# Performance work log

Measured on AMD Instinct MI355X. Metric: run time of the kernel, lower is better.

Reference implementation:

```python
import jax, jax.numpy as jnp
import numpy as np

N_USERS = 100000
M_ITEMS = 200000
K_DIM = 128
N_BASKET = 50
GAMMA = (1.0, 1.0, 1.0, 1.0)


def setup_inputs() -> dict:
    key = jax.random.key(0)
    k1, k2, k3, k4, k5 = jax.random.split(key, 5)
    n, m, k = N_USERS, M_ITEMS, K_DIM
    p = n + 2 * m
    # Build one transaction x of length 2*p: [target transaction t | t^m transaction]
    rng = np.random.default_rng(0)
    x = np.zeros(2 * p, dtype=np.float32)
    # target transaction t
    x[rng.integers(n)] = 1.0                      # user one-hot
    x[n + rng.integers(m)] = 1.0                  # target item one-hot
    basket = rng.choice(m, size=N_BASKET, replace=False)
    x[n + m + basket] = 1.0                       # basket multi-hot
    # t^m transaction (unused by forward math, present for faithfulness)
    x[p + rng.integers(n)] = 1.0
    x[p + n + rng.integers(m)] = 1.0
    basket2 = rng.choice(m, size=N_BASKET, replace=False)
    x[p + n + m + basket2] = 1.0
    return {
        "x": jnp.asarray(x),
        "delta": jnp.ones((1,), dtype=jnp.float32),
        "pmi": jnp.zeros((1,), dtype=jnp.float32),
        "w_0": jax.random.normal(k1, (1,), dtype=jnp.float32),
        "w_bias": jax.random.normal(k2, (p, 1), dtype=jnp.float32),
        "u_V": jax.random.normal(k3, (n, k), dtype=jnp.float32),
        "t_V": jax.random.normal(k4, (m, k), dtype=jnp.float32),
        "b_V": jax.random.normal(k5, (m, k), dtype=jnp.float32),
    }


def _fm(t, w_0, w_bias, u_V, t_V, b_V):
    n, m = u_V.shape[0], t_V.shape[0]
    xr = t[None, :]                                  # (1, n+2m)
    bias = xr @ w_bias                               # (1, 1)
    u_vec = xr[:, :n] @ u_V                          # (1, k) user latent
    t_vec = xr[:, n:n + m] @ t_V                     # (1, k) target-item latent
    xb = t[n + m:]                                   # (m,) basket multi-hot mask
    s = xb @ b_V                                     # (k,)  sum of selected basket vecs
    sq_sum = jnp.sum(xb @ (b_V * b_V))               # scalar sum_i ||b_i||^2
    u_t = jnp.sum(u_vec * t_vec, axis=-1, keepdims=True)   # (1,1)
    t_b = jnp.sum(t_vec * s, axis=-1, keepdims=True)        # (1,1) sum_i t.b_i
    # closed-form FM pairwise trick: sum_{i<j} b_i.b_j = 0.5*(||sum||^2 - sum ||.||^2)
    bs = 0.5 * (jnp.sum(s * s) - sq_sum)                    # scalar
    u_b = jnp.sum(u_vec * s, axis=-1, keepdims=True)        # (1,1)
    g0, g1, g2, g3 = GAMMA
    return w_0 + bias + g0 * u_t + g1 * t_b + g2 * bs + g3 * u_b


def reference(x, delta, pmi, w_0, w_bias, u_V, t_V, b_V):
    n, m = u_V.shape[0], t_V.shape[0]
    p = n + 2 * m
    t = x[:p]
    y = _fm(t, w_0, w_bias, u_V, t_V, b_V)           # (1,1)
    y = -jax.nn.log_sigmoid(y * delta)
    return y
```

## Files before the change

### kernel.cpp

```cpp
#include <hip/hip_runtime.h>
#include <math.h>

#define N_USERS 100000
#define M_ITEMS 200000
#define K_DIM   128
#define P_DIM   (N_USERS + 2 * M_ITEMS)
#define CAP     1024


__global__ void scan_kernel(const float* __restrict__ x,
                            int* __restrict__ count,
                            int* __restrict__ eidx,
                            float* __restrict__ eval) {
    const int n4 = P_DIM / 4;
    int i4 = blockIdx.x * blockDim.x + threadIdx.x;
    if (i4 >= n4) return;
    float4 v = reinterpret_cast<const float4*>(x)[i4];
    float a0 = v.x, a1 = v.y, a2 = v.z, a3 = v.w;
    if (a0 != 0.0f) { int p = atomicAdd(count, 1); if (p < CAP) { eidx[p] = 4*i4 + 0; eval[p] = a0; } }
    if (a1 != 0.0f) { int p = atomicAdd(count, 1); if (p < CAP) { eidx[p] = 4*i4 + 1; eval[p] = a1; } }
    if (a2 != 0.0f) { int p = atomicAdd(count, 1); if (p < CAP) { eidx[p] = 4*i4 + 2; eval[p] = a2; } }
    if (a3 != 0.0f) { int p = atomicAdd(count, 1); if (p < CAP) { eidx[p] = 4*i4 + 3; eval[p] = a3; } }
}

__global__ void finish_kernel(const int* __restrict__ count,
                              const int* __restrict__ eidx,
                              const float* __restrict__ eval,
                              const float* __restrict__ w0,
                              const float* __restrict__ delta,
                              const float* __restrict__ w_bias,
                              const float* __restrict__ uV,
                              const float* __restrict__ tV,
                              const float* __restrict__ bV,
                              float* __restrict__ out) {
    const int tid = threadIdx.x;
    int cnt = *count;
    if (cnt > CAP) cnt = CAP;

    float u = 0.0f, t = 0.0f, s = 0.0f, sq = 0.0f, bias = 0.0f;
    for (int e = 0; e < cnt; ++e) {
        const int   idx = eidx[e];
        const float val = eval[e];
        if (tid == 0) bias += val * w_bias[idx];
        if (idx < N_USERS) {
            u += val * uV[(size_t)idx * K_DIM + tid];
        } else if (idx < N_USERS + M_ITEMS) {
            t += val * tV[(size_t)(idx - N_USERS) * K_DIM + tid];
        } else {
            float b = bV[(size_t)(idx - N_USERS - M_ITEMS) * K_DIM + tid];
            s  += val * b;
            sq += val * b * b;
        }
    }

    __shared__ float sh[5][K_DIM];
    sh[0][tid] = u * t;
    sh[1][tid] = t * s;
    sh[2][tid] = s * s;
    sh[3][tid] = u * s;
    sh[4][tid] = sq;
    __syncthreads();
    for (int off = K_DIM / 2; off > 0; off >>= 1) {
        if (tid < off) {
            #pragma unroll
            for (int j = 0; j < 5; ++j) sh[j][tid] += sh[j][tid + off];
        }
        __syncthreads();
    }

    if (tid == 0) {
        const float ut = sh[0][0], tb = sh[1][0], ss = sh[2][0],
                    ub = sh[3][0], sqs = sh[4][0];
        const float bs = 0.5f * (ss - sqs);
        float y = w0[0] + bias + ut + tb + bs + ub;
        float z = y * delta[0];
        float a = -z;
        out[0] = fmaxf(a, 0.0f) + log1pf(expf(-fabsf(a)));
    }
}

extern "C" void kernel_launch(void* const* d_in, const int* in_sizes, int n_in,
                              void* d_out, int out_size, void* d_ws, size_t ws_size,
                              hipStream_t stream) {
    const float* x      = (const float*)d_in[0];
    const float* delta  = (const float*)d_in[1];
    const float* w0     = (const float*)d_in[3];
    const float* w_bias = (const float*)d_in[4];
    const float* uV     = (const float*)d_in[5];
    const float* tV     = (const float*)d_in[6];
    const float* bV     = (const float*)d_in[7];
    float* out = (float*)d_out;

    int*   count = (int*)d_ws;
    int*   eidx  = (int*)((char*)d_ws + 16);
    float* eval  = (float*)((char*)d_ws + 16 + CAP * sizeof(int));

    hipMemsetAsync(d_ws, 0, 16, stream);

    const int n4 = P_DIM / 4;
    const int blocks = (n4 + 255) / 256;
    scan_kernel<<<blocks, 256, 0, stream>>>(x, count, eidx, eval);
    finish_kernel<<<1, K_DIM, 0, stream>>>(count, eidx, eval, w0, delta,
                                           w_bias, uV, tV, bV, out);
}
```

Baseline: 250.0 us.

## Compact nonzeros per block in LDS and parallelize gather across 1024 threads

The scan kernel now collects nonzeros into a per-block shared-memory list and writes per-block counts, so the global atomic counter and the memset launch are no longer needed. The finish kernel gathers these per-block lists into shared memory, then splits the embedding-row gathers across 8 slices of 128 threads and computes the bias terms in parallel with a tree reduction. This targets the serial latency chain of the single 128-thread finish loop and removes global atomics. In exchange, the finish kernel must read all per-block counts, and nonzeros beyond the fixed per-block and total caps are dropped.

```diff
diff --git a/kernel.cpp b/kernel.cpp
--- a/kernel.cpp
+++ b/kernel.cpp
@@ -5,74 +5,134 @@
 #define M_ITEMS 200000
 #define K_DIM   128
 #define P_DIM   (N_USERS + 2 * M_ITEMS)
-#define CAP     1024
+#define N4      (P_DIM / 4)
+#define SCAN_T  256
+#define SCAN_BLOCKS ((N4 + SCAN_T - 1) / SCAN_T)
+#define SLOTS   64
+#define MAXNZ   256
 
 
-__global__ void scan_kernel(const float* __restrict__ x,
-                            int* __restrict__ count,
-                            int* __restrict__ eidx,
-                            float* __restrict__ eval) {
-    const int n4 = P_DIM / 4;
-    int i4 = blockIdx.x * blockDim.x + threadIdx.x;
-    if (i4 >= n4) return;
-    float4 v = reinterpret_cast<const float4*>(x)[i4];
-    float a0 = v.x, a1 = v.y, a2 = v.z, a3 = v.w;
-    if (a0 != 0.0f) { int p = atomicAdd(count, 1); if (p < CAP) { eidx[p] = 4*i4 + 0; eval[p] = a0; } }
-    if (a1 != 0.0f) { int p = atomicAdd(count, 1); if (p < CAP) { eidx[p] = 4*i4 + 1; eval[p] = a1; } }
-    if (a2 != 0.0f) { int p = atomicAdd(count, 1); if (p < CAP) { eidx[p] = 4*i4 + 2; eval[p] = a2; } }
-    if (a3 != 0.0f) { int p = atomicAdd(count, 1); if (p < CAP) { eidx[p] = 4*i4 + 3; eval[p] = a3; } }
+__global__ __launch_bounds__(SCAN_T) void scan_kernel(
+        const float* __restrict__ x,
+        int* __restrict__ counts,
+        int* __restrict__ gidx,
+        float* __restrict__ gval) {
+    __shared__ int lc;
+    __shared__ int   lidx[SLOTS];
+    __shared__ float lval[SLOTS];
+    const int tid = threadIdx.x;
+    const int b   = blockIdx.x;
+    if (tid == 0) lc = 0;
+    __syncthreads();
+
+    const int i4 = b * SCAN_T + tid;
+    if (i4 < N4) {
+        float4 v = reinterpret_cast<const float4*>(x)[i4];
+        float a[4] = {v.x, v.y, v.z, v.w};
+        #pragma unroll
+        for (int j = 0; j < 4; ++j) {
+            if (a[j] != 0.0f) {
+                int p = atomicAdd(&lc, 1);
+                if (p < SLOTS) { lidx[p] = 4 * i4 + j; lval[p] = a[j]; }
+            }
+        }
+    }
+    __syncthreads();
+    int c = lc; if (c > SLOTS) c = SLOTS;
+    if (tid == 0) counts[b] = c;
+    if (tid < c) {
+        gidx[b * SLOTS + tid] = lidx[tid];
+        gval[b * SLOTS + tid] = lval[tid];
+    }
 }
 
-__global__ void finish_kernel(const int* __restrict__ count,
-                              const int* __restrict__ eidx,
-                              const float* __restrict__ eval,
-                              const float* __restrict__ w0,
-                              const float* __restrict__ delta,
-                              const float* __restrict__ w_bias,
-                              const float* __restrict__ uV,
-                              const float* __restrict__ tV,
-                              const float* __restrict__ bV,
-                              float* __restrict__ out) {
+__global__ __launch_bounds__(1024) void finish_kernel(
+        const int* __restrict__ counts,
+        const int* __restrict__ gidx,
+        const float* __restrict__ gval,
+        const float* __restrict__ w0,
+        const float* __restrict__ delta,
+        const float* __restrict__ w_bias,
+        const float* __restrict__ uV,
+        const float* __restrict__ tV,
+        const float* __restrict__ bV,
+        float* __restrict__ out) {
     const int tid = threadIdx.x;
-    int cnt = *count;
-    if (cnt > CAP) cnt = CAP;
 
-    float u = 0.0f, t = 0.0f, s = 0.0f, sq = 0.0f, bias = 0.0f;
-    for (int e = 0; e < cnt; ++e) {
-        const int   idx = eidx[e];
-        const float val = eval[e];
-        if (tid == 0) bias += val * w_bias[idx];
+    __shared__ int   lcnt;
+    __shared__ int   lidx[MAXNZ];
+    __shared__ float lval[MAXNZ];
+    __shared__ float sb[MAXNZ];
+    __shared__ float pu[8][K_DIM], pt[8][K_DIM], ps[8][K_DIM], psq[8][K_DIM];
+    __shared__ float red[5][K_DIM];
+
+    if (tid == 0) lcnt = 0;
+    __syncthreads();
+
+    if (tid < SCAN_BLOCKS) {
+        int cb = counts[tid];
+        for (int j = 0; j < cb; ++j) {
+            int p = atomicAdd(&lcnt, 1);
+            if (p < MAXNZ) {
+                lidx[p] = gidx[tid * SLOTS + j];
+                lval[p] = gval[tid * SLOTS + j];
+            }
+        }
+    }
+    __syncthreads();
+    int cnt = lcnt; if (cnt > MAXNZ) cnt = MAXNZ;
+
+    if (tid < MAXNZ)
+        sb[tid] = (tid < cnt) ? lval[tid] * w_bias[lidx[tid]] : 0.0f;
+
+    const int k  = tid & (K_DIM - 1);
+    const int sl = tid >> 7;
+    float u = 0.0f, t = 0.0f, s = 0.0f, sq = 0.0f;
+    for (int e = sl; e < cnt; e += 8) {
+        const int   idx = lidx[e];
+        const float val = lval[e];
         if (idx < N_USERS) {
-            u += val * uV[(size_t)idx * K_DIM + tid];
+            u += val * uV[(size_t)idx * K_DIM + k];
         } else if (idx < N_USERS + M_ITEMS) {
-            t += val * tV[(size_t)(idx - N_USERS) * K_DIM + tid];
+            t += val * tV[(size_t)(idx - N_USERS) * K_DIM + k];
         } else {
-            float b = bV[(size_t)(idx - N_USERS - M_ITEMS) * K_DIM + tid];
+            float b = bV[(size_t)(idx - N_USERS - M_ITEMS) * K_DIM + k];
             s  += val * b;
             sq += val * b * b;
         }
     }
+    pu[sl][k] = u; pt[sl][k] = t; ps[sl][k] = s; psq[sl][k] = sq;
+    __syncthreads();
 
-    __shared__ float sh[5][K_DIM];
-    sh[0][tid] = u * t;
-    sh[1][tid] = t * s;
-    sh[2][tid] = s * s;
-    sh[3][tid] = u * s;
-    sh[4][tid] = sq;
+    if (tid < K_DIM) {
+        float U = 0.0f, T = 0.0f, S = 0.0f, SQ = 0.0f;
+        #pragma unroll
+        for (int j = 0; j < 8; ++j) {
+            U += pu[j][tid]; T += pt[j][tid]; S += ps[j][tid]; SQ += psq[j][tid];
+        }
+        red[0][tid] = U * T;
+        red[1][tid] = T * S;
+        red[2][tid] = S * S;
+        red[3][tid] = U * S;
+        red[4][tid] = SQ;
+    }
+    __syncthreads();
+    if (tid < 128) sb[tid] += sb[tid + 128];
     __syncthreads();
     for (int off = K_DIM / 2; off > 0; off >>= 1) {
         if (tid < off) {
             #pragma unroll
-            for (int j = 0; j < 5; ++j) sh[j][tid] += sh[j][tid + off];
+            for (int j = 0; j < 5; ++j) red[j][tid] += red[j][tid + off];
+            sb[tid] += sb[tid + off];
         }
         __syncthreads();
     }
 
     if (tid == 0) {
-        const float ut = sh[0][0], tb = sh[1][0], ss = sh[2][0],
-                    ub = sh[3][0], sqs = sh[4][0];
+        const float ut = red[0][0], tb = red[1][0], ss = red[2][0],
+                    ub = red[3][0], sqs = red[4][0];
         const float bs = 0.5f * (ss - sqs);
-        float y = w0[0] + bias + ut + tb + bs + ub;
+        float y = w0[0] + sb[0] + ut + tb + bs + ub;
         float z = y * delta[0];
         float a = -z;
         out[0] = fmaxf(a, 0.0f) + log1pf(expf(-fabsf(a)));
@@ -91,15 +151,11 @@
     const float* bV     = (const float*)d_in[7];
     float* out = (float*)d_out;
 
-    int*   count = (int*)d_ws;
-    int*   eidx  = (int*)((char*)d_ws + 16);
-    float* eval  = (float*)((char*)d_ws + 16 + CAP * sizeof(int));
+    int*   counts = (int*)d_ws;
+    int*   gidx   = (int*)((char*)d_ws + 4096);
+    float* gval   = (float*)((char*)d_ws + 4096 + SCAN_BLOCKS * SLOTS * sizeof(int));
 
-    hipMemsetAsync(d_ws, 0, 16, stream);
-
-    const int n4 = P_DIM / 4;
-    const int blocks = (n4 + 255) / 256;
-    scan_kernel<<<blocks, 256, 0, stream>>>(x, count, eidx, eval);
-    finish_kernel<<<1, K_DIM, 0, stream>>>(count, eidx, eval, w0, delta,
-                                           w_bias, uV, tV, bV, out);
+    scan_kernel<<<SCAN_BLOCKS, SCAN_T, 0, stream>>>(x, counts, gidx, gval);
+    finish_kernel<<<1, 1024, 0, stream>>>(counts, gidx, gval, w0, delta,
+                                          w_bias, uV, tV, bV, out);
 }
```

After: 207.8 us. 16.9% less time.
